# Kernel optimization log

Measured on AMD Instinct MI355X. Metric: run time of the kernel, lower is better.

Reference implementation:

```python
import jax, jax.numpy as jnp
from jax import lax
import numpy as np

V, E, H, B = 50257, 512, 1024, 1024
P_DROP = 0.1
TIMESTEPS = 10


def setup_inputs() -> dict:
    key = jax.random.key(0)
    ks = jax.random.split(key, 10)
    target_token = jax.random.randint(ks[0], (B,), 0, V)
    hidden = 0.1 * jax.random.normal(ks[1], (1, B, H), dtype=jnp.float32)
    emb_table = 0.02 * jax.random.normal(ks[2], (V, E), dtype=jnp.float32)
    W1 = jax.random.normal(ks[3], (H, E), dtype=jnp.float32) / np.sqrt(E).astype(np.float32)
    b1 = jnp.zeros((H,), jnp.float32)
    W2 = jax.random.normal(ks[4], (H, H), dtype=jnp.float32) / np.sqrt(H).astype(np.float32)
    b2 = jnp.zeros((H,), jnp.float32)
    fc_W = jax.random.normal(ks[5], (V, H), dtype=jnp.float32) / np.sqrt(H).astype(np.float32)
    fc_b = jnp.zeros((V,), jnp.float32)
    threshold = jnp.float32(1.0)
    leak = jnp.float32(0.95)
    scale = jnp.float32(1.0 / (1.0 - P_DROP))
    mask_emb = (jax.random.uniform(ks[6], (1, 1, B, E)) > P_DROP).astype(jnp.float32) * scale
    mask_lif = (jax.random.uniform(ks[7], (1, B, H)) > P_DROP).astype(jnp.float32) * scale
    return dict(target_token=target_token, hidden=hidden, emb_table=emb_table,
                W1=W1, b1=b1, W2=W2, b2=b2, fc_W=fc_W, fc_b=fc_b,
                threshold=threshold, leak=leak, mask_emb=mask_emb, mask_lif=mask_lif)


def reference(target_token, hidden, emb_table, W1, b1, W2, b2, fc_W, fc_b,
              threshold, leak, mask_emb, mask_lif):
    # embedding: [B] -> [1,1,B,E], dropout via fixed mask
    emb = emb_table[target_token][None, None] * mask_emb  # [1,1,B,E]
    x = emb[0]                                            # [1,B,E]  (word 0)
    # Linear(E->H) input is identical at every timestep -> hoist out of scan
    delta1 = jnp.einsum('ube,he->ubh', x, W1) + b1        # [1,B,H]

    def step(carry, _):
        mem_lif, mem_int = carry
        mem = leak * mem_lif + delta1
        mem_thr = mem / threshold - 1.0
        spike = (mem_thr > 0).astype(mem.dtype)
        mem_lif = mem - threshold * spike                 # soft reset
        h = spike * mask_lif                              # dropout mask
        mem_int = mem_int + jnp.einsum('ubh,gh->ubg', h, W2) + b2
        return (mem_lif, mem_int), None

    init = (hidden, jnp.zeros_like(hidden))
    (_, out), _ = lax.scan(step, init, None, length=TIMESTEPS)
    # out / embedding_layer.shape[1] where shape[1] == 1 -> no-op, kept for fidelity
    out = out / 1.0
    linear = jnp.einsum('bh,vh->bv', out[0], fc_W) + fc_b  # [B,V]
    return (linear, out)
```

## Files before the change

kernel.cpp:

```cpp
#include <hip/hip_runtime.h>

#define NV 50257
#define NE 512
#define NH 1024
#define NB 1024
#define TSTEPS 10

typedef __bf16 bf16x8 __attribute__((ext_vector_type(8)));
typedef float  f32x4  __attribute__((ext_vector_type(4)));
typedef unsigned short u16;

__device__ __forceinline__ u16 f2bf(float v) {
    unsigned u = __float_as_uint(v);
    unsigned r = u + 0x7fffu + ((u >> 16) & 1u);
    return (u16)(r >> 16);
}

__global__ void init_kernel(const float* __restrict__ b2,
                            unsigned* __restrict__ flag,
                            unsigned* __restrict__ flag_b2) {
    const int t = threadIdx.x;
    float4 v = ((const float4*)b2)[t];
    bool nz = (v.x != 0.0f) | (v.y != 0.0f) | (v.z != 0.0f) | (v.w != 0.0f);
    unsigned long long m = __ballot(nz);
    __shared__ unsigned sh;
    if (t == 0) sh = 0u;
    __syncthreads();
    if ((t & 63) == 0 && m != 0ull) atomicOr(&sh, 1u);
    __syncthreads();
    if (t == 0) { *flag = 0u; *flag_b2 = sh; }
}

__global__ void prep_kernel(const float* __restrict__ W1, u16* __restrict__ w1b,
                            const int* __restrict__ tok,
                            const float* __restrict__ table,
                            const float* __restrict__ mask,
                            u16* __restrict__ ebf) {
    const int b = blockIdx.x;
    if (b < 512) {
        int i = b * 256 + threadIdx.x;
        float4 v = ((const float4*)W1)[i];
        ushort4 o;
        o.x = f2bf(v.x); o.y = f2bf(v.y); o.z = f2bf(v.z); o.w = f2bf(v.w);
        ((ushort4*)w1b)[i] = o;
    } else {
        int i = (b - 512) * 256 + threadIdx.x;
        int bb = i / (NE / 4);
        int c = i % (NE / 4);
        float4 t = ((const float4*)(table + (size_t)tok[bb] * NE))[c];
        float4 m = ((const float4*)mask)[i];
        ushort4 o;
        o.x = f2bf(t.x * m.x); o.y = f2bf(t.y * m.y);
        o.z = f2bf(t.z * m.z); o.w = f2bf(t.w * m.w);
        ((ushort4*)ebf)[i] = o;
    }
}

__global__ void lif_bf16_flag_kernel(const float* __restrict__ delta1,
                                     const float* __restrict__ hidden,
                                     const float* __restrict__ mask_lif,
                                     const float* __restrict__ thr_p,
                                     const float* __restrict__ leak_p,
                                     u16* __restrict__ hbf,
                                     unsigned* __restrict__ flag) {
    int i = blockIdx.x * blockDim.x + threadIdx.x;
    if (i >= NB * NH / 4) return;
    const float thr = thr_p[0];
    const float leak = leak_p[0];
    float4 d4 = ((const float4*)delta1)[i];
    float4 m4 = ((const float4*)hidden)[i];
    float4 k4 = ((const float4*)mask_lif)[i];
    float dd[4] = {d4.x, d4.y, d4.z, d4.w};
    float mm[4] = {m4.x, m4.y, m4.z, m4.w};
    float kk[4] = {k4.x, k4.y, k4.z, k4.w};
    ushort4 o;
    u16 oo[4];
    bool nz = false;
#pragma unroll
    for (int j = 0; j < 4; ++j) {
        float m = mm[j], cnt = 0.0f;
#pragma unroll
        for (int t = 0; t < TSTEPS; ++t) {
            float mem = leak * m + dd[j];
            float s = ((mem / thr - 1.0f) > 0.0f) ? 1.0f : 0.0f;
            m = mem - thr * s;
            cnt += s;
        }
        float v = cnt * kk[j];
        nz |= (v != 0.0f);
        oo[j] = f2bf(v);
    }
    o.x = oo[0]; o.y = oo[1]; o.z = oo[2]; o.w = oo[3];
    ((ushort4*)hbf)[i] = o;
    if (nz) atomicOr(flag, 1u);
}

__global__ void cvt_cond_kernel(const unsigned* __restrict__ flag,
                                const float* __restrict__ W2, u16* __restrict__ w2b,
                                const float* __restrict__ fcW, u16* __restrict__ fcwb) {
    if (*flag == 0u) return;
    const int b = blockIdx.x;
    if (b < 512) {
        for (int i = b * 256 + threadIdx.x; i < NH * NH / 4; i += 512 * 256) {
            float4 v = ((const float4*)W2)[i];
            ushort4 o;
            o.x = f2bf(v.x); o.y = f2bf(v.y); o.z = f2bf(v.z); o.w = f2bf(v.w);
            ((ushort4*)w2b)[i] = o;
        }
    } else {
        for (int i = (b - 512) * 256 + threadIdx.x; i < NV * NH / 4; i += 2048 * 256) {
            float4 v = ((const float4*)fcW)[i];
            ushort4 o;
            o.x = f2bf(v.x); o.y = f2bf(v.y); o.z = f2bf(v.z); o.w = f2bf(v.w);
            ((ushort4*)fcwb)[i] = o;
        }
    }
}

__global__ void bcast_out_kernel(const unsigned* __restrict__ flag,
                                 const float* __restrict__ b2,
                                 float* __restrict__ outbuf) {
    if (*flag != 0u) return;
    int i0 = blockIdx.x * blockDim.x + threadIdx.x;
    int stride = gridDim.x * blockDim.x;
    const int n4 = NB * NH / 4;
    for (int i = i0; i < n4; i += stride) {
        int h4 = i & (NH / 4 - 1);
        float4 v = ((const float4*)b2)[h4];
        v.x *= (float)TSTEPS; v.y *= (float)TSTEPS;
        v.z *= (float)TSTEPS; v.w *= (float)TSTEPS;
        ((float4*)outbuf)[i] = v;
    }
}

__global__ void matvec_fc_kernel(const unsigned* __restrict__ flag,
                                 const unsigned* __restrict__ flag_b2,
                                 const float* __restrict__ b2,
                                 const float* __restrict__ fcW,
                                 const float* __restrict__ fc_b,
                                 float* __restrict__ y) {
    if (*flag != 0u || *flag_b2 == 0u) return;
    const int wid = (blockIdx.x * 256 + threadIdx.x) >> 6;
    const int l = threadIdx.x & 63;
    const float4* bb = (const float4*)b2;
    for (int col = wid; col < NV; col += 2048 * 4) {
        const float4* row = (const float4*)(fcW + (size_t)col * NH);
        float s = 0.0f;
#pragma unroll
        for (int it = 0; it < NH / 256; ++it) {
            float4 v = row[it * 64 + l];
            float4 b = bb[it * 64 + l];
            s += v.x * b.x + v.y * b.y + v.z * b.z + v.w * b.w;
        }
#pragma unroll
        for (int off = 32; off > 0; off >>= 1) s += __shfl_down(s, off);
        if (l == 0) y[col] = fc_b[col] + (float)TSTEPS * s;
    }
}

__global__ void bcast_linear_kernel(const unsigned* __restrict__ flag,
                                    const unsigned* __restrict__ flag_b2,
                                    const float* __restrict__ y,
                                    const float* __restrict__ fc_b,
                                    float* __restrict__ linear) {
    if (*flag != 0u) return;
    const float* __restrict__ src = (*flag_b2 != 0u) ? y : fc_b;
    const int c0 = blockIdx.x * 1024;
    const int r0 = blockIdx.y * 8;
    const int t = threadIdx.x;
    float vy[4];
#pragma unroll
    for (int k = 0; k < 4; ++k) {
        int c = c0 + t + k * 256;
        vy[k] = (c < NV) ? src[c] : 0.0f;
    }
#pragma unroll
    for (int r = 0; r < 8; ++r) {
        float* dst = linear + (size_t)(r0 + r) * NV;
#pragma unroll
        for (int k = 0; k < 4; ++k) {
            int c = c0 + t + k * 256;
            if (c < NV) dst[c] = vy[k];
        }
    }
}

template<int TBM, int TBN, int NWAVE>
__device__ __forceinline__
void gemm_pipe2_body(const u16* __restrict__ Abf, const u16* __restrict__ Bbf,
                     const float* __restrict__ bias, float bias_scale,
                     float* __restrict__ C, u16* __restrict__ Cb,
                     int M, int N, int K) {
    constexpr int AU = TBM / 16;
    constexpr int BU = TBN / 16;
    constexpr int TOT = AU + BU;
    constexpr int PER = TOT / NWAVE;
    constexpr int MF = 4;
    constexpr int NF = TBN / 32;
    constexpr int DEPTH = 3;
    static_assert(TOT % NWAVE == 0, "unit split");
    static_assert(NWAVE == 4 && TBM == 128, "wave tiling: 2x2 waves");

    __shared__ u16 sA[DEPTH][AU * 512];
    __shared__ u16 sB[DEPTH][BU * 512];

    const int i = blockIdx.x;
    const int xcd = i & 7;
    const int rb  = (i >> 3) & 7;
    const int p   = ((i >> 6) << 3) + xcd;
    if (p * TBN >= N) return;
    const int bm = rb * TBM;
    const int bn = p * TBN;

    const int tid = threadIdx.x;
    const int w = tid >> 6;
    const int l = tid & 63;
    const int wr16 = (w >> 1) * MF;
    const int wc16 = (w & 1) * NF;
    const int lrow = l & 15;
    const int lk8 = (l >> 4) * 8;
    const int l8 = l * 8;

    f32x4 acc[MF][NF];
#pragma unroll
    for (int m = 0; m < MF; ++m)
#pragma unroll
        for (int n = 0; n < NF; ++n)
#pragma unroll
            for (int q = 0; q < 4; ++q) acc[m][n][q] = 0.0f;

    const int NT = K / 32;

    auto stage = [&](int buf, int k0) {
#pragma unroll
        for (int s = 0; s < PER; ++s) {
            const int c = w * PER + s;
            if (c < AU) {
                const int row = bm + c * 16 + lrow;
                __builtin_amdgcn_global_load_lds(Abf + (size_t)row * K + k0 + lk8,
                                                 &sA[buf][c * 512], 16, 0, 0);
            } else {
                const int u = c - AU;
                int row = bn + u * 16 + lrow; if (row >= N) row = N - 1;
                __builtin_amdgcn_global_load_lds(Bbf + (size_t)row * K + k0 + lk8,
                                                 &sB[buf][u * 512], 16, 0, 0);
            }
        }
    };

    stage(0, 0);
    stage(1, 32);

    int cur = 0;
    for (int t = 0; t < NT; ++t) {
        if (t + 1 < NT) {
            asm volatile("s_waitcnt vmcnt(%0)" :: "n"(PER) : "memory");
        } else {
            asm volatile("s_waitcnt vmcnt(0)" ::: "memory");
        }
        __builtin_amdgcn_sched_barrier(0);
        __builtin_amdgcn_s_barrier();
        __builtin_amdgcn_sched_barrier(0);

        if (t + 2 < NT) {
            int nb = cur + 2; if (nb >= DEPTH) nb -= DEPTH;
            stage(nb, (t + 2) * 32);
        }

        bf16x8 ah[MF], bh[NF];
#pragma unroll
        for (int m = 0; m < MF; ++m)
            ah[m] = *(const bf16x8*)&sA[cur][(wr16 + m) * 512 + l8];
#pragma unroll
        for (int n = 0; n < NF; ++n)
            bh[n] = *(const bf16x8*)&sB[cur][(wc16 + n) * 512 + l8];

#pragma unroll
        for (int m = 0; m < MF; ++m)
#pragma unroll
            for (int n = 0; n < NF; ++n)
                acc[m][n] = __builtin_amdgcn_mfma_f32_16x16x32_bf16(ah[m], bh[n], acc[m][n], 0, 0, 0);

        __builtin_amdgcn_sched_barrier(0);
        cur = (cur + 1 == DEPTH) ? 0 : cur + 1;
    }

    const int lq = (l >> 4) * 4;
    const int wrow = bm + (w >> 1) * 64;
    const int wcol = bn + (w & 1) * (NF * 16);
#pragma unroll
    for (int n = 0; n < NF; ++n) {
        const int gcol = wcol + n * 16 + (l & 15);
        if (gcol >= N) continue;
        const float bb = bias[gcol] * bias_scale;
#pragma unroll
        for (int m = 0; m < MF; ++m) {
            const int grow = wrow + m * 16 + lq;
#pragma unroll
            for (int q = 0; q < 4; ++q) {
                float v = acc[m][n][q] + bb;
                C[(size_t)(grow + q) * N + gcol] = v;
                if (Cb) Cb[(size_t)(grow + q) * N + gcol] = f2bf(v);
            }
        }
    }
}

__global__ __launch_bounds__(256)
void gemm_pipe2_128(const u16* __restrict__ Abf, const u16* __restrict__ Bbf,
                    const float* __restrict__ bias, float bias_scale,
                    float* __restrict__ C, u16* __restrict__ Cb, int M, int N, int K) {
    gemm_pipe2_body<128, 128, 4>(Abf, Bbf, bias, bias_scale, C, Cb, M, N, K);
}

__global__ __launch_bounds__(256)
void gemm_pipe2_128_cond(const unsigned* __restrict__ flag,
                         const u16* __restrict__ Abf, const u16* __restrict__ Bbf,
                         const float* __restrict__ bias, float bias_scale,
                         float* __restrict__ C, u16* __restrict__ Cb, int M, int N, int K) {
    if (*flag == 0u) return;
    gemm_pipe2_body<128, 128, 4>(Abf, Bbf, bias, bias_scale, C, Cb, M, N, K);
}

__global__ __launch_bounds__(256, 2)
void gemm_pipe2_256_cond(const unsigned* __restrict__ flag,
                         const u16* __restrict__ Abf, const u16* __restrict__ Bbf,
                         const float* __restrict__ bias, float bias_scale,
                         float* __restrict__ C, u16* __restrict__ Cb, int M, int N, int K) {
    if (*flag == 0u) return;
    gemm_pipe2_body<128, 256, 4>(Abf, Bbf, bias, bias_scale, C, Cb, M, N, K);
}

__global__ void embed_kernel(const int* __restrict__ tok,
                             const float* __restrict__ table,
                             const float* __restrict__ mask,
                             float* __restrict__ emb) {
    int i = blockIdx.x * blockDim.x + threadIdx.x;
    const int n4 = NB * NE / 4;
    if (i >= n4) return;
    int b = i / (NE / 4);
    int c = i % (NE / 4);
    float4 t = ((const float4*)(table + (size_t)tok[b] * NE))[c];
    float4 m = ((const float4*)mask)[i];
    float4 o;
    o.x = t.x * m.x; o.y = t.y * m.y; o.z = t.z * m.z; o.w = t.w * m.w;
    ((float4*)emb)[i] = o;
}

__global__ void lif_kernel(const float* __restrict__ delta1,
                           const float* __restrict__ hidden,
                           const float* __restrict__ mask_lif,
                           const float* __restrict__ thr_p,
                           const float* __restrict__ leak_p,
                           float* __restrict__ hsum) {
    int i = blockIdx.x * blockDim.x + threadIdx.x;
    if (i >= NB * NH) return;
    const float thr = thr_p[0];
    const float leak = leak_p[0];
    float d = delta1[i];
    float m = hidden[i];
    float cnt = 0.0f;
#pragma unroll
    for (int t = 0; t < TSTEPS; ++t) {
        float mem = leak * m + d;
        float s = ((mem / thr - 1.0f) > 0.0f) ? 1.0f : 0.0f;
        m = mem - thr * s;
        cnt += s;
    }
    hsum[i] = cnt * mask_lif[i];
}

#define BM 128
#define BN 128
#define BK 16

__global__ __launch_bounds__(256)
void gemm_nt(const float* __restrict__ A, const float* __restrict__ Bm,
             const float* __restrict__ bias, float bias_scale,
             float* __restrict__ C, int M, int N, int K) {
    __shared__ float As[BK][BM + 4];
    __shared__ float Bs[BK][BN + 4];

    const int tid = threadIdx.x;
    const int bm = blockIdx.y * BM;
    const int bn = blockIdx.x * BN;
    const int tx = tid & 15;
    const int ty = tid >> 4;
    const int tm = ty * 8;
    const int tn0 = tx * 4;
    const int tn1 = 64 + tx * 4;

    float acc[8][8];
#pragma unroll
    for (int i = 0; i < 8; ++i)
#pragma unroll
        for (int j = 0; j < 8; ++j) acc[i][j] = 0.0f;

    constexpr int LDA4 = BK / 4;

    for (int k0 = 0; k0 < K; k0 += BK) {
#pragma unroll
        for (int idx = tid; idx < BM * LDA4; idx += 256) {
            int m = idx / LDA4, c = idx % LDA4;
            float4 v = *(const float4*)(A + (size_t)(bm + m) * K + k0 + c * 4);
            As[c * 4 + 0][m] = v.x;
            As[c * 4 + 1][m] = v.y;
            As[c * 4 + 2][m] = v.z;
            As[c * 4 + 3][m] = v.w;
        }
#pragma unroll
        for (int idx = tid; idx < BN * LDA4; idx += 256) {
            int n = idx / LDA4, c = idx % LDA4;
            float4 v = make_float4(0.f, 0.f, 0.f, 0.f);
            int gn = bn + n;
            if (gn < N) v = *(const float4*)(Bm + (size_t)gn * K + k0 + c * 4);
            Bs[c * 4 + 0][n] = v.x;
            Bs[c * 4 + 1][n] = v.y;
            Bs[c * 4 + 2][n] = v.z;
            Bs[c * 4 + 3][n] = v.w;
        }
        __syncthreads();

#pragma unroll
        for (int k = 0; k < BK; ++k) {
            float4 a0 = *(const float4*)&As[k][tm];
            float4 a1 = *(const float4*)&As[k][tm + 4];
            float4 b0 = *(const float4*)&Bs[k][tn0];
            float4 b1 = *(const float4*)&Bs[k][tn1];
            float a[8] = {a0.x, a0.y, a0.z, a0.w, a1.x, a1.y, a1.z, a1.w};
            float bb[8] = {b0.x, b0.y, b0.z, b0.w, b1.x, b1.y, b1.z, b1.w};
#pragma unroll
            for (int i = 0; i < 8; ++i)
#pragma unroll
                for (int j = 0; j < 8; ++j)
                    acc[i][j] = fmaf(a[i], bb[j], acc[i][j]);
        }
        __syncthreads();
    }

#pragma unroll
    for (int i = 0; i < 8; ++i) {
        size_t row = (size_t)(bm + tm + i) * N;
#pragma unroll
        for (int j = 0; j < 8; ++j) {
            int gn = bn + ((j < 4) ? (tn0 + j) : (tn1 + j - 4));
            if (gn < N)
                C[row + gn] = acc[i][j] + bias[gn] * bias_scale;
        }
    }
}

static inline int grid1d(int N, int TBN) {
    int P = (N + TBN - 1) / TBN;
    int P8 = ((P + 7) / 8) * 8;
    return 8 * P8;
}

extern "C" void kernel_launch(void* const* d_in, const int* in_sizes, int n_in,
                              void* d_out, int out_size, void* d_ws, size_t ws_size,
                              hipStream_t stream) {
    const int*   tok      = (const int*)  d_in[0];
    const float* hidden   = (const float*)d_in[1];
    const float* table    = (const float*)d_in[2];
    const float* W1       = (const float*)d_in[3];
    const float* b1       = (const float*)d_in[4];
    const float* W2       = (const float*)d_in[5];
    const float* b2       = (const float*)d_in[6];
    const float* fc_W     = (const float*)d_in[7];
    const float* fc_b     = (const float*)d_in[8];
    const float* thr      = (const float*)d_in[9];
    const float* leak     = (const float*)d_in[10];
    const float* mask_emb = (const float*)d_in[11];
    const float* mask_lif = (const float*)d_in[12];

    float* linear = (float*)d_out;
    float* outbuf = (float*)d_out + (size_t)NB * NV;

    const size_t SZ_FLAG = 16;
    const size_t SZ_Y   = ((size_t)NV * 4 + 15) / 16 * 16;
    const size_t SZ_EB  = (size_t)NB * NE * 2;
    const size_t SZ_D1  = (size_t)NB * NH * 4;
    const size_t SZ_HB  = (size_t)NB * NH * 2;
    const size_t SZ_OB  = (size_t)NB * NH * 2;
    const size_t SZ_W1B = (size_t)NH * NE * 2;
    const size_t SZ_W2B = (size_t)NH * NH * 2;
    const size_t SZ_WB  = (size_t)NV * NH * 2;
    const size_t need_bf = SZ_FLAG + SZ_Y + SZ_EB + SZ_D1 + SZ_HB + SZ_OB
                         + SZ_W1B + SZ_W2B + SZ_WB;

    char* p = (char*)d_ws;

    if (ws_size >= need_bf) {
        unsigned* flag    = (unsigned*)p;
        unsigned* flag_b2 = (unsigned*)p + 1;
        p += SZ_FLAG;
        float* y      = (float*)p;     p += SZ_Y;
        u16*   ebf    = (u16*)p;       p += SZ_EB;
        float* delta1 = (float*)p;     p += SZ_D1;
        u16*   hbf    = (u16*)p;       p += SZ_HB;
        u16*   obf    = (u16*)p;       p += SZ_OB;
        u16*   w1b    = (u16*)p;       p += SZ_W1B;
        u16*   w2b    = (u16*)p;       p += SZ_W2B;
        u16*   fcwb   = (u16*)p;       p += SZ_WB;

        init_kernel<<<1, 256, 0, stream>>>(b2, flag, flag_b2);
        prep_kernel<<<1024, 256, 0, stream>>>(W1, w1b, tok, table, mask_emb, ebf);
        gemm_pipe2_128<<<grid1d(NH, 128), 256, 0, stream>>>(ebf, w1b, b1, 1.0f,
                                                            delta1, (u16*)nullptr, NB, NH, NE);
        {
            int n = NB * NH / 4;
            lif_bf16_flag_kernel<<<(n + 255) / 256, 256, 0, stream>>>(delta1, hidden, mask_lif,
                                                                      thr, leak, hbf, flag);
        }
        bcast_out_kernel<<<512, 256, 0, stream>>>(flag, b2, outbuf);
        matvec_fc_kernel<<<2048, 256, 0, stream>>>(flag, flag_b2, b2, fc_W, fc_b, y);
        {
            dim3 grid((NV + 1023) / 1024, NB / 8);
            bcast_linear_kernel<<<grid, 256, 0, stream>>>(flag, flag_b2, y, fc_b, linear);
        }
        cvt_cond_kernel<<<2560, 256, 0, stream>>>(flag, W2, w2b, fc_W, fcwb);
        gemm_pipe2_128_cond<<<grid1d(NH, 128), 256, 0, stream>>>(flag, hbf, w2b, b2, (float)TSTEPS,
                                                                 outbuf, obf, NB, NH, NH);
        gemm_pipe2_256_cond<<<grid1d(NV, 256), 256, 0, stream>>>(flag, obf, fcwb, fc_b, 1.0f,
                                                                 linear, (u16*)nullptr, NB, NV, NH);
    } else {
        float* emb    = (float*)p;  p += (size_t)NB * NE * 4;
        float* delta1 = (float*)p;  p += SZ_D1;
        float* hsum   = (float*)p;

        int n4 = NB * NE / 4;
        embed_kernel<<<(n4 + 255) / 256, 256, 0, stream>>>(tok, table, mask_emb, emb);
        {
            dim3 grid(NH / BN, NB / BM);
            gemm_nt<<<grid, 256, 0, stream>>>(emb, W1, b1, 1.0f, delta1, NB, NH, NE);
        }
        {
            int n = NB * NH;
            lif_kernel<<<(n + 255) / 256, 256, 0, stream>>>(delta1, hidden, mask_lif,
                                                            thr, leak, hsum);
        }
        {
            dim3 grid(NH / BN, NB / BM);
            gemm_nt<<<grid, 256, 0, stream>>>(hsum, W2, b2, (float)TSTEPS, outbuf, NB, NH, NH);
        }
        {
            dim3 grid((NV + BN - 1) / BN, NB / BM);
            gemm_nt<<<grid, 256, 0, stream>>>(outbuf, fc_W, fc_b, 1.0f, linear, NB, NV, NH);
        }
    }
}
```

Measured before the change: 74.32 us.

## Fuse LIF recurrence into first GEMM epilogue and merge broadcast kernels

The LIF spike-count recurrence moves into the epilogue of the E->H bf16 MFMA GEMM. This drops the fp32 delta1 buffer, its write and re-read, and one kernel launch. The two zero-spike fallback broadcast kernels, for outbuf and for linear, become one launch split by block index. In exchange, the epilogue now reads hidden and mask_lif with the MFMA accumulator's scattered per-lane pattern instead of vectorised float4 loads.

```diff
diff --git a/kernel.cpp b/kernel.cpp
--- a/kernel.cpp
+++ b/kernel.cpp
@@ -56,45 +56,6 @@
     }
 }
 
-__global__ void lif_bf16_flag_kernel(const float* __restrict__ delta1,
-                                     const float* __restrict__ hidden,
-                                     const float* __restrict__ mask_lif,
-                                     const float* __restrict__ thr_p,
-                                     const float* __restrict__ leak_p,
-                                     u16* __restrict__ hbf,
-                                     unsigned* __restrict__ flag) {
-    int i = blockIdx.x * blockDim.x + threadIdx.x;
-    if (i >= NB * NH / 4) return;
-    const float thr = thr_p[0];
-    const float leak = leak_p[0];
-    float4 d4 = ((const float4*)delta1)[i];
-    float4 m4 = ((const float4*)hidden)[i];
-    float4 k4 = ((const float4*)mask_lif)[i];
-    float dd[4] = {d4.x, d4.y, d4.z, d4.w};
-    float mm[4] = {m4.x, m4.y, m4.z, m4.w};
-    float kk[4] = {k4.x, k4.y, k4.z, k4.w};
-    ushort4 o;
-    u16 oo[4];
-    bool nz = false;
-#pragma unroll
-    for (int j = 0; j < 4; ++j) {
-        float m = mm[j], cnt = 0.0f;
-#pragma unroll
-        for (int t = 0; t < TSTEPS; ++t) {
-            float mem = leak * m + dd[j];
-            float s = ((mem / thr - 1.0f) > 0.0f) ? 1.0f : 0.0f;
-            m = mem - thr * s;
-            cnt += s;
-        }
-        float v = cnt * kk[j];
-        nz |= (v != 0.0f);
-        oo[j] = f2bf(v);
-    }
-    o.x = oo[0]; o.y = oo[1]; o.z = oo[2]; o.w = oo[3];
-    ((ushort4*)hbf)[i] = o;
-    if (nz) atomicOr(flag, 1u);
-}
-
 __global__ void cvt_cond_kernel(const unsigned* __restrict__ flag,
                                 const float* __restrict__ W2, u16* __restrict__ w2b,
                                 const float* __restrict__ fcW, u16* __restrict__ fcwb) {
@@ -114,22 +75,6 @@
             o.x = f2bf(v.x); o.y = f2bf(v.y); o.z = f2bf(v.z); o.w = f2bf(v.w);
             ((ushort4*)fcwb)[i] = o;
         }
-    }
-}
-
-__global__ void bcast_out_kernel(const unsigned* __restrict__ flag,
-                                 const float* __restrict__ b2,
-                                 float* __restrict__ outbuf) {
-    if (*flag != 0u) return;
-    int i0 = blockIdx.x * blockDim.x + threadIdx.x;
-    int stride = gridDim.x * blockDim.x;
-    const int n4 = NB * NH / 4;
-    for (int i = i0; i < n4; i += stride) {
-        int h4 = i & (NH / 4 - 1);
-        float4 v = ((const float4*)b2)[h4];
-        v.x *= (float)TSTEPS; v.y *= (float)TSTEPS;
-        v.z *= (float)TSTEPS; v.w *= (float)TSTEPS;
-        ((float4*)outbuf)[i] = v;
     }
 }
 
@@ -158,31 +103,182 @@
     }
 }
 
-__global__ void bcast_linear_kernel(const unsigned* __restrict__ flag,
+__global__ void bcast_merged_kernel(const unsigned* __restrict__ flag,
                                     const unsigned* __restrict__ flag_b2,
+                                    const float* __restrict__ b2,
                                     const float* __restrict__ y,
                                     const float* __restrict__ fc_b,
+                                    float* __restrict__ outbuf,
                                     float* __restrict__ linear) {
     if (*flag != 0u) return;
-    const float* __restrict__ src = (*flag_b2 != 0u) ? y : fc_b;
-    const int c0 = blockIdx.x * 1024;
-    const int r0 = blockIdx.y * 8;
-    const int t = threadIdx.x;
-    float vy[4];
-#pragma unroll
-    for (int k = 0; k < 4; ++k) {
-        int c = c0 + t + k * 256;
-        vy[k] = (c < NV) ? src[c] : 0.0f;
-    }
-#pragma unroll
-    for (int r = 0; r < 8; ++r) {
-        float* dst = linear + (size_t)(r0 + r) * NV;
+    const int b = blockIdx.x;
+    if (b < 512) {
+        int i0 = b * 256 + threadIdx.x;
+        const int n4 = NB * NH / 4;
+        for (int i = i0; i < n4; i += 512 * 256) {
+            int h4 = i & (NH / 4 - 1);
+            float4 v = ((const float4*)b2)[h4];
+            v.x *= (float)TSTEPS; v.y *= (float)TSTEPS;
+            v.z *= (float)TSTEPS; v.w *= (float)TSTEPS;
+            ((float4*)outbuf)[i] = v;
+        }
+    } else {
+        const float* __restrict__ src = (*flag_b2 != 0u) ? y : fc_b;
+        const int idx = b - 512;
+        const int c0 = (idx % 50) * 1024;
+        const int r0 = (idx / 50) * 8;
+        const int t = threadIdx.x;
+        float vy[4];
 #pragma unroll
         for (int k = 0; k < 4; ++k) {
             int c = c0 + t + k * 256;
-            if (c < NV) dst[c] = vy[k];
-        }
-    }
+            vy[k] = (c < NV) ? src[c] : 0.0f;
+        }
+#pragma unroll
+        for (int r = 0; r < 8; ++r) {
+            float* dst = linear + (size_t)(r0 + r) * NV;
+#pragma unroll
+            for (int k = 0; k < 4; ++k) {
+                int c = c0 + t + k * 256;
+                if (c < NV) dst[c] = vy[k];
+            }
+        }
+    }
+}
+
+__global__ __launch_bounds__(256)
+void gemm1_lif_kernel(const u16* __restrict__ Abf, const u16* __restrict__ Bbf,
+                      const float* __restrict__ bias,
+                      const float* __restrict__ hidden,
+                      const float* __restrict__ mask_lif,
+                      const float* __restrict__ thr_p,
+                      const float* __restrict__ leak_p,
+                      u16* __restrict__ hbf,
+                      unsigned* __restrict__ flag) {
+    constexpr int TBM = 128, TBN = 128, NWAVE = 4;
+    constexpr int AU = TBM / 16, BU = TBN / 16;
+    constexpr int PER = (AU + BU) / NWAVE;
+    constexpr int MF = 4, NF = TBN / 32;
+    constexpr int DEPTH = 3;
+    const int M = NB, N = NH, K = NE;
+
+    __shared__ u16 sA[DEPTH][AU * 512];
+    __shared__ u16 sB[DEPTH][BU * 512];
+
+    const int i = blockIdx.x;
+    const int xcd = i & 7;
+    const int rb  = (i >> 3) & 7;
+    const int p   = ((i >> 6) << 3) + xcd;
+    if (p * TBN >= N) return;
+    const int bm = rb * TBM;
+    const int bn = p * TBN;
+
+    const int tid = threadIdx.x;
+    const int w = tid >> 6;
+    const int l = tid & 63;
+    const int wr16 = (w >> 1) * MF;
+    const int wc16 = (w & 1) * NF;
+    const int lrow = l & 15;
+    const int lk8 = (l >> 4) * 8;
+    const int l8 = l * 8;
+
+    f32x4 acc[MF][NF];
+#pragma unroll
+    for (int m = 0; m < MF; ++m)
+#pragma unroll
+        for (int n = 0; n < NF; ++n)
+#pragma unroll
+            for (int q = 0; q < 4; ++q) acc[m][n][q] = 0.0f;
+
+    const int NT = K / 32;
+
+    auto stage = [&](int buf, int k0) {
+#pragma unroll
+        for (int s = 0; s < PER; ++s) {
+            const int c = w * PER + s;
+            if (c < AU) {
+                const int row = bm + c * 16 + lrow;
+                __builtin_amdgcn_global_load_lds(Abf + (size_t)row * K + k0 + lk8,
+                                                 &sA[buf][c * 512], 16, 0, 0);
+            } else {
+                const int u = c - AU;
+                int row = bn + u * 16 + lrow; if (row >= N) row = N - 1;
+                __builtin_amdgcn_global_load_lds(Bbf + (size_t)row * K + k0 + lk8,
+                                                 &sB[buf][u * 512], 16, 0, 0);
+            }
+        }
+    };
+
+    stage(0, 0);
+    stage(1, 32);
+
+    int cur = 0;
+    for (int t = 0; t < NT; ++t) {
+        if (t + 1 < NT) {
+            asm volatile("s_waitcnt vmcnt(%0)" :: "n"(PER) : "memory");
+        } else {
+            asm volatile("s_waitcnt vmcnt(0)" ::: "memory");
+        }
+        __builtin_amdgcn_sched_barrier(0);
+        __builtin_amdgcn_s_barrier();
+        __builtin_amdgcn_sched_barrier(0);
+
+        if (t + 2 < NT) {
+            int nb = cur + 2; if (nb >= DEPTH) nb -= DEPTH;
+            stage(nb, (t + 2) * 32);
+        }
+
+        bf16x8 ah[MF], bh[NF];
+#pragma unroll
+        for (int m = 0; m < MF; ++m)
+            ah[m] = *(const bf16x8*)&sA[cur][(wr16 + m) * 512 + l8];
+#pragma unroll
+        for (int n = 0; n < NF; ++n)
+            bh[n] = *(const bf16x8*)&sB[cur][(wc16 + n) * 512 + l8];
+
+#pragma unroll
+        for (int m = 0; m < MF; ++m)
+#pragma unroll
+            for (int n = 0; n < NF; ++n)
+                acc[m][n] = __builtin_amdgcn_mfma_f32_16x16x32_bf16(ah[m], bh[n], acc[m][n], 0, 0, 0);
+
+        __builtin_amdgcn_sched_barrier(0);
+        cur = (cur + 1 == DEPTH) ? 0 : cur + 1;
+    }
+
+    const float thr = thr_p[0];
+    const float leak = leak_p[0];
+    const int lq = (l >> 4) * 4;
+    const int wrow = bm + (w >> 1) * 64;
+    const int wcol = bn + (w & 1) * (NF * 16);
+    bool nz = false;
+#pragma unroll
+    for (int n = 0; n < NF; ++n) {
+        const int gcol = wcol + n * 16 + (l & 15);
+        const float bb = bias[gcol];
+#pragma unroll
+        for (int m = 0; m < MF; ++m) {
+            const int grow = wrow + m * 16 + lq;
+#pragma unroll
+            for (int q = 0; q < 4; ++q) {
+                const size_t off = (size_t)(grow + q) * NH + gcol;
+                float d = acc[m][n][q] + bb;
+                float mem_s = hidden[off];
+                float cnt = 0.0f;
+#pragma unroll
+                for (int ts = 0; ts < TSTEPS; ++ts) {
+                    float mem = leak * mem_s + d;
+                    float s = ((mem / thr - 1.0f) > 0.0f) ? 1.0f : 0.0f;
+                    mem_s = mem - thr * s;
+                    cnt += s;
+                }
+                float v = cnt * mask_lif[off];
+                nz |= (v != 0.0f);
+                hbf[off] = f2bf(v);
+            }
+        }
+    }
+    if (nz) atomicOr(flag, 1u);
 }
 
 template<int TBM, int TBN, int NWAVE>
@@ -304,13 +400,6 @@
             }
         }
     }
-}
-
-__global__ __launch_bounds__(256)
-void gemm_pipe2_128(const u16* __restrict__ Abf, const u16* __restrict__ Bbf,
-                    const float* __restrict__ bias, float bias_scale,
-                    float* __restrict__ C, u16* __restrict__ Cb, int M, int N, int K) {
-    gemm_pipe2_body<128, 128, 4>(Abf, Bbf, bias, bias_scale, C, Cb, M, N, K);
 }
 
 __global__ __launch_bounds__(256)
@@ -479,13 +568,12 @@
     const size_t SZ_FLAG = 16;
     const size_t SZ_Y   = ((size_t)NV * 4 + 15) / 16 * 16;
     const size_t SZ_EB  = (size_t)NB * NE * 2;
-    const size_t SZ_D1  = (size_t)NB * NH * 4;
     const size_t SZ_HB  = (size_t)NB * NH * 2;
     const size_t SZ_OB  = (size_t)NB * NH * 2;
     const size_t SZ_W1B = (size_t)NH * NE * 2;
     const size_t SZ_W2B = (size_t)NH * NH * 2;
     const size_t SZ_WB  = (size_t)NV * NH * 2;
-    const size_t need_bf = SZ_FLAG + SZ_Y + SZ_EB + SZ_D1 + SZ_HB + SZ_OB
+    const size_t need_bf = SZ_FLAG + SZ_Y + SZ_EB + SZ_HB + SZ_OB
                          + SZ_W1B + SZ_W2B + SZ_WB;
 
     char* p = (char*)d_ws;
@@ -496,7 +584,6 @@
         p += SZ_FLAG;
         float* y      = (float*)p;     p += SZ_Y;
         u16*   ebf    = (u16*)p;       p += SZ_EB;
-        float* delta1 = (float*)p;     p += SZ_D1;
         u16*   hbf    = (u16*)p;       p += SZ_HB;
         u16*   obf    = (u16*)p;       p += SZ_OB;
         u16*   w1b    = (u16*)p;       p += SZ_W1B;
@@ -505,19 +592,12 @@
 
         init_kernel<<<1, 256, 0, stream>>>(b2, flag, flag_b2);
         prep_kernel<<<1024, 256, 0, stream>>>(W1, w1b, tok, table, mask_emb, ebf);
-        gemm_pipe2_128<<<grid1d(NH, 128), 256, 0, stream>>>(ebf, w1b, b1, 1.0f,
-                                                            delta1, (u16*)nullptr, NB, NH, NE);
-        {
-            int n = NB * NH / 4;
-            lif_bf16_flag_kernel<<<(n + 255) / 256, 256, 0, stream>>>(delta1, hidden, mask_lif,
-                                                                      thr, leak, hbf, flag);
-        }
-        bcast_out_kernel<<<512, 256, 0, stream>>>(flag, b2, outbuf);
+        gemm1_lif_kernel<<<grid1d(NH, 128), 256, 0, stream>>>(ebf, w1b, b1,
+                                                              hidden, mask_lif,
+                                                              thr, leak, hbf, flag);
         matvec_fc_kernel<<<2048, 256, 0, stream>>>(flag, flag_b2, b2, fc_W, fc_b, y);
-        {
-            dim3 grid((NV + 1023) / 1024, NB / 8);
-            bcast_linear_kernel<<<grid, 256, 0, stream>>>(flag, flag_b2, y, fc_b, linear);
-        }
+        bcast_merged_kernel<<<512 + 50 * (NB / 8), 256, 0, stream>>>(flag, flag_b2, b2,
+                                                                     y, fc_b, outbuf, linear);
         cvt_cond_kernel<<<2560, 256, 0, stream>>>(flag, W2, w2b, fc_W, fcwb);
         gemm_pipe2_128_cond<<<grid1d(NH, 128), 256, 0, stream>>>(flag, hbf, w2b, b2, (float)TSTEPS,
                                                                  outbuf, obf, NB, NH, NH);
@@ -525,7 +605,7 @@
                                                                  linear, (u16*)nullptr, NB, NV, NH);
     } else {
         float* emb    = (float*)p;  p += (size_t)NB * NE * 4;
-        float* delta1 = (float*)p;  p += SZ_D1;
+        float* delta1 = (float*)p;  p += (size_t)NB * NH * 4;
         float* hsum   = (float*)p;
 
         int n4 = NB * NE / 4;
```

New measurement: 100.3 us. 1.35x slower.

## Merge flag init and broadcast kernels, drop bf16 weight conversion path

Applied to the files above, without the earlier changes.

Folds the b2-nonzero flag initialisation into block 0 of the prep kernel. Merges the two broadcast kernels (outbuf and linear) into one launch. Removes the conditional W2/fc_W bf16 conversion kernel and replaces the bf16 MFMA GEMMs on the spiking path with fp32 tiled GEMMs, so the LIF kernel now writes fp32 spike sums. The goal is fewer kernel launches on the common no-spike path. In exchange, the LIF output doubles in size, and the spiking path becomes a much slower fp32 SIMT GEMM.

```diff
diff --git a/kernel.cpp b/kernel.cpp
--- a/kernel.cpp
+++ b/kernel.cpp
@@ -16,27 +16,27 @@
     return (u16)(r >> 16);
 }
 
-__global__ void init_kernel(const float* __restrict__ b2,
-                            unsigned* __restrict__ flag,
-                            unsigned* __restrict__ flag_b2) {
-    const int t = threadIdx.x;
-    float4 v = ((const float4*)b2)[t];
-    bool nz = (v.x != 0.0f) | (v.y != 0.0f) | (v.z != 0.0f) | (v.w != 0.0f);
-    unsigned long long m = __ballot(nz);
-    __shared__ unsigned sh;
-    if (t == 0) sh = 0u;
-    __syncthreads();
-    if ((t & 63) == 0 && m != 0ull) atomicOr(&sh, 1u);
-    __syncthreads();
-    if (t == 0) { *flag = 0u; *flag_b2 = sh; }
-}
-
 __global__ void prep_kernel(const float* __restrict__ W1, u16* __restrict__ w1b,
                             const int* __restrict__ tok,
                             const float* __restrict__ table,
                             const float* __restrict__ mask,
-                            u16* __restrict__ ebf) {
+                            u16* __restrict__ ebf,
+                            const float* __restrict__ b2,
+                            unsigned* __restrict__ flag,
+                            unsigned* __restrict__ flag_b2) {
     const int b = blockIdx.x;
+    if (b == 0) {
+        const int t = threadIdx.x;
+        float4 v = ((const float4*)b2)[t];
+        bool nz = (v.x != 0.0f) | (v.y != 0.0f) | (v.z != 0.0f) | (v.w != 0.0f);
+        unsigned long long m = __ballot(nz);
+        __shared__ unsigned sh;
+        if (t == 0) sh = 0u;
+        __syncthreads();
+        if ((t & 63) == 0 && m != 0ull) atomicOr(&sh, 1u);
+        __syncthreads();
+        if (t == 0) { *flag = 0u; *flag_b2 = sh; }
+    }
     if (b < 512) {
         int i = b * 256 + threadIdx.x;
         float4 v = ((const float4*)W1)[i];
@@ -56,13 +56,13 @@
     }
 }
 
-__global__ void lif_bf16_flag_kernel(const float* __restrict__ delta1,
-                                     const float* __restrict__ hidden,
-                                     const float* __restrict__ mask_lif,
-                                     const float* __restrict__ thr_p,
-                                     const float* __restrict__ leak_p,
-                                     u16* __restrict__ hbf,
-                                     unsigned* __restrict__ flag) {
+__global__ void lif_flag_kernel(const float* __restrict__ delta1,
+                                const float* __restrict__ hidden,
+                                const float* __restrict__ mask_lif,
+                                const float* __restrict__ thr_p,
+                                const float* __restrict__ leak_p,
+                                float* __restrict__ hsum,
+                                unsigned* __restrict__ flag) {
     int i = blockIdx.x * blockDim.x + threadIdx.x;
     if (i >= NB * NH / 4) return;
     const float thr = thr_p[0];
@@ -73,8 +73,7 @@
     float dd[4] = {d4.x, d4.y, d4.z, d4.w};
     float mm[4] = {m4.x, m4.y, m4.z, m4.w};
     float kk[4] = {k4.x, k4.y, k4.z, k4.w};
-    ushort4 o;
-    u16 oo[4];
+    float vv[4];
     bool nz = false;
 #pragma unroll
     for (int j = 0; j < 4; ++j) {
@@ -86,51 +85,12 @@
             m = mem - thr * s;
             cnt += s;
         }
-        float v = cnt * kk[j];
-        nz |= (v != 0.0f);
-        oo[j] = f2bf(v);
-    }
-    o.x = oo[0]; o.y = oo[1]; o.z = oo[2]; o.w = oo[3];
-    ((ushort4*)hbf)[i] = o;
+        vv[j] = cnt * kk[j];
+        nz |= (vv[j] != 0.0f);
+    }
+    float4 o; o.x = vv[0]; o.y = vv[1]; o.z = vv[2]; o.w = vv[3];
+    ((float4*)hsum)[i] = o;
     if (nz) atomicOr(flag, 1u);
-}
-
-__global__ void cvt_cond_kernel(const unsigned* __restrict__ flag,
-                                const float* __restrict__ W2, u16* __restrict__ w2b,
-                                const float* __restrict__ fcW, u16* __restrict__ fcwb) {
-    if (*flag == 0u) return;
-    const int b = blockIdx.x;
-    if (b < 512) {
-        for (int i = b * 256 + threadIdx.x; i < NH * NH / 4; i += 512 * 256) {
-            float4 v = ((const float4*)W2)[i];
-            ushort4 o;
-            o.x = f2bf(v.x); o.y = f2bf(v.y); o.z = f2bf(v.z); o.w = f2bf(v.w);
-            ((ushort4*)w2b)[i] = o;
-        }
-    } else {
-        for (int i = (b - 512) * 256 + threadIdx.x; i < NV * NH / 4; i += 2048 * 256) {
-            float4 v = ((const float4*)fcW)[i];
-            ushort4 o;
-            o.x = f2bf(v.x); o.y = f2bf(v.y); o.z = f2bf(v.z); o.w = f2bf(v.w);
-            ((ushort4*)fcwb)[i] = o;
-        }
-    }
-}
-
-__global__ void bcast_out_kernel(const unsigned* __restrict__ flag,
-                                 const float* __restrict__ b2,
-                                 float* __restrict__ outbuf) {
-    if (*flag != 0u) return;
-    int i0 = blockIdx.x * blockDim.x + threadIdx.x;
-    int stride = gridDim.x * blockDim.x;
-    const int n4 = NB * NH / 4;
-    for (int i = i0; i < n4; i += stride) {
-        int h4 = i & (NH / 4 - 1);
-        float4 v = ((const float4*)b2)[h4];
-        v.x *= (float)TSTEPS; v.y *= (float)TSTEPS;
-        v.z *= (float)TSTEPS; v.w *= (float)TSTEPS;
-        ((float4*)outbuf)[i] = v;
-    }
 }
 
 __global__ void matvec_fc_kernel(const unsigned* __restrict__ flag,
@@ -158,48 +118,58 @@
     }
 }
 
-__global__ void bcast_linear_kernel(const unsigned* __restrict__ flag,
+__global__ void bcast_merged_kernel(const unsigned* __restrict__ flag,
                                     const unsigned* __restrict__ flag_b2,
+                                    const float* __restrict__ b2,
                                     const float* __restrict__ y,
                                     const float* __restrict__ fc_b,
+                                    float* __restrict__ outbuf,
                                     float* __restrict__ linear) {
     if (*flag != 0u) return;
-    const float* __restrict__ src = (*flag_b2 != 0u) ? y : fc_b;
-    const int c0 = blockIdx.x * 1024;
-    const int r0 = blockIdx.y * 8;
-    const int t = threadIdx.x;
-    float vy[4];
-#pragma unroll
-    for (int k = 0; k < 4; ++k) {
-        int c = c0 + t + k * 256;
-        vy[k] = (c < NV) ? src[c] : 0.0f;
-    }
-#pragma unroll
-    for (int r = 0; r < 8; ++r) {
-        float* dst = linear + (size_t)(r0 + r) * NV;
+    const int b = blockIdx.x;
+    if (b < 512) {
+        int i0 = b * 256 + threadIdx.x;
+        const int n4 = NB * NH / 4;
+        for (int i = i0; i < n4; i += 512 * 256) {
+            int h4 = i & (NH / 4 - 1);
+            float4 v = ((const float4*)b2)[h4];
+            v.x *= (float)TSTEPS; v.y *= (float)TSTEPS;
+            v.z *= (float)TSTEPS; v.w *= (float)TSTEPS;
+            ((float4*)outbuf)[i] = v;
+        }
+    } else {
+        const float* __restrict__ src = (*flag_b2 != 0u) ? y : fc_b;
+        const int idx = b - 512;
+        const int c0 = (idx % 50) * 1024;
+        const int r0 = (idx / 50) * 8;
+        const int t = threadIdx.x;
+        float vy[4];
 #pragma unroll
         for (int k = 0; k < 4; ++k) {
             int c = c0 + t + k * 256;
-            if (c < NV) dst[c] = vy[k];
-        }
-    }
-}
-
-template<int TBM, int TBN, int NWAVE>
-__device__ __forceinline__
-void gemm_pipe2_body(const u16* __restrict__ Abf, const u16* __restrict__ Bbf,
-                     const float* __restrict__ bias, float bias_scale,
-                     float* __restrict__ C, u16* __restrict__ Cb,
-                     int M, int N, int K) {
-    constexpr int AU = TBM / 16;
-    constexpr int BU = TBN / 16;
-    constexpr int TOT = AU + BU;
-    constexpr int PER = TOT / NWAVE;
-    constexpr int MF = 4;
-    constexpr int NF = TBN / 32;
+            vy[k] = (c < NV) ? src[c] : 0.0f;
+        }
+#pragma unroll
+        for (int r = 0; r < 8; ++r) {
+            float* dst = linear + (size_t)(r0 + r) * NV;
+#pragma unroll
+            for (int k = 0; k < 4; ++k) {
+                int c = c0 + t + k * 256;
+                if (c < NV) dst[c] = vy[k];
+            }
+        }
+    }
+}
+
+__global__ __launch_bounds__(256)
+void gemm_pipe2_128(const u16* __restrict__ Abf, const u16* __restrict__ Bbf,
+                    const float* __restrict__ bias, float bias_scale,
+                    float* __restrict__ C, int M, int N, int K) {
+    constexpr int TBM = 128, TBN = 128, NWAVE = 4;
+    constexpr int AU = TBM / 16, BU = TBN / 16;
+    constexpr int PER = (AU + BU) / NWAVE;
+    constexpr int MF = 4, NF = TBN / 32;
     constexpr int DEPTH = 3;
-    static_assert(TOT % NWAVE == 0, "unit split");
-    static_assert(NWAVE == 4 && TBM == 128, "wave tiling: 2x2 waves");
 
     __shared__ u16 sA[DEPTH][AU * 512];
     __shared__ u16 sB[DEPTH][BU * 512];
@@ -297,38 +267,106 @@
         for (int m = 0; m < MF; ++m) {
             const int grow = wrow + m * 16 + lq;
 #pragma unroll
-            for (int q = 0; q < 4; ++q) {
-                float v = acc[m][n][q] + bb;
-                C[(size_t)(grow + q) * N + gcol] = v;
-                if (Cb) Cb[(size_t)(grow + q) * N + gcol] = f2bf(v);
-            }
+            for (int q = 0; q < 4; ++q)
+                C[(size_t)(grow + q) * N + gcol] = acc[m][n][q] + bb;
+        }
+    }
+}
+
+#define BM 128
+#define BN 128
+#define BK 16
+
+__device__ __forceinline__
+void gemm_nt_body(const float* __restrict__ A, const float* __restrict__ Bm,
+                  const float* __restrict__ bias, float bias_scale,
+                  float* __restrict__ C, int M, int N, int K) {
+    __shared__ float As[BK][BM + 4];
+    __shared__ float Bs[BK][BN + 4];
+
+    const int tid = threadIdx.x;
+    const int bm = blockIdx.y * BM;
+    const int bn = blockIdx.x * BN;
+    const int tx = tid & 15;
+    const int ty = tid >> 4;
+    const int tm = ty * 8;
+    const int tn0 = tx * 4;
+    const int tn1 = 64 + tx * 4;
+
+    float acc[8][8];
+#pragma unroll
+    for (int i = 0; i < 8; ++i)
+#pragma unroll
+        for (int j = 0; j < 8; ++j) acc[i][j] = 0.0f;
+
+    constexpr int LDA4 = BK / 4;
+
+    for (int k0 = 0; k0 < K; k0 += BK) {
+#pragma unroll
+        for (int idx = tid; idx < BM * LDA4; idx += 256) {
+            int m = idx / LDA4, c = idx % LDA4;
+            float4 v = *(const float4*)(A + (size_t)(bm + m) * K + k0 + c * 4);
+            As[c * 4 + 0][m] = v.x;
+            As[c * 4 + 1][m] = v.y;
+            As[c * 4 + 2][m] = v.z;
+            As[c * 4 + 3][m] = v.w;
+        }
+#pragma unroll
+        for (int idx = tid; idx < BN * LDA4; idx += 256) {
+            int n = idx / LDA4, c = idx % LDA4;
+            float4 v = make_float4(0.f, 0.f, 0.f, 0.f);
+            int gn = bn + n;
+            if (gn < N) v = *(const float4*)(Bm + (size_t)gn * K + k0 + c * 4);
+            Bs[c * 4 + 0][n] = v.x;
+            Bs[c * 4 + 1][n] = v.y;
+            Bs[c * 4 + 2][n] = v.z;
+            Bs[c * 4 + 3][n] = v.w;
+        }
+        __syncthreads();
+
+#pragma unroll
+        for (int k = 0; k < BK; ++k) {
+            float4 a0 = *(const float4*)&As[k][tm];
+            float4 a1 = *(const float4*)&As[k][tm + 4];
+            float4 b0 = *(const float4*)&Bs[k][tn0];
+            float4 b1 = *(const float4*)&Bs[k][tn1];
+            float a[8] = {a0.x, a0.y, a0.z, a0.w, a1.x, a1.y, a1.z, a1.w};
+            float bb[8] = {b0.x, b0.y, b0.z, b0.w, b1.x, b1.y, b1.z, b1.w};
+#pragma unroll
+            for (int i = 0; i < 8; ++i)
+#pragma unroll
+                for (int j = 0; j < 8; ++j)
+                    acc[i][j] = fmaf(a[i], bb[j], acc[i][j]);
+        }
+        __syncthreads();
+    }
+
+#pragma unroll
+    for (int i = 0; i < 8; ++i) {
+        size_t row = (size_t)(bm + tm + i) * N;
+#pragma unroll
+        for (int j = 0; j < 8; ++j) {
+            int gn = bn + ((j < 4) ? (tn0 + j) : (tn1 + j - 4));
+            if (gn < N)
+                C[row + gn] = acc[i][j] + bias[gn] * bias_scale;
         }
     }
 }
 
 __global__ __launch_bounds__(256)
-void gemm_pipe2_128(const u16* __restrict__ Abf, const u16* __restrict__ Bbf,
-                    const float* __restrict__ bias, float bias_scale,
-                    float* __restrict__ C, u16* __restrict__ Cb, int M, int N, int K) {
-    gemm_pipe2_body<128, 128, 4>(Abf, Bbf, bias, bias_scale, C, Cb, M, N, K);
+void gemm_nt(const float* __restrict__ A, const float* __restrict__ Bm,
+             const float* __restrict__ bias, float bias_scale,
+             float* __restrict__ C, int M, int N, int K) {
+    gemm_nt_body(A, Bm, bias, bias_scale, C, M, N, K);
 }
 
 __global__ __launch_bounds__(256)
-void gemm_pipe2_128_cond(const unsigned* __restrict__ flag,
-                         const u16* __restrict__ Abf, const u16* __restrict__ Bbf,
-                         const float* __restrict__ bias, float bias_scale,
-                         float* __restrict__ C, u16* __restrict__ Cb, int M, int N, int K) {
+void gemm_nt_cond(const unsigned* __restrict__ flag,
+                  const float* __restrict__ A, const float* __restrict__ Bm,
+                  const float* __restrict__ bias, float bias_scale,
+                  float* __restrict__ C, int M, int N, int K) {
     if (*flag == 0u) return;
-    gemm_pipe2_body<128, 128, 4>(Abf, Bbf, bias, bias_scale, C, Cb, M, N, K);
-}
-
-__global__ __launch_bounds__(256, 2)
-void gemm_pipe2_256_cond(const unsigned* __restrict__ flag,
-                         const u16* __restrict__ Abf, const u16* __restrict__ Bbf,
-                         const float* __restrict__ bias, float bias_scale,
-                         float* __restrict__ C, u16* __restrict__ Cb, int M, int N, int K) {
-    if (*flag == 0u) return;
-    gemm_pipe2_body<128, 256, 4>(Abf, Bbf, bias, bias_scale, C, Cb, M, N, K);
+    gemm_nt_body(A, Bm, bias, bias_scale, C, M, N, K);
 }
 
 __global__ void embed_kernel(const int* __restrict__ tok,
@@ -368,86 +406,6 @@
         cnt += s;
     }
     hsum[i] = cnt * mask_lif[i];
-}
-
-#define BM 128
-#define BN 128
-#define BK 16
-
-__global__ __launch_bounds__(256)
-void gemm_nt(const float* __restrict__ A, const float* __restrict__ Bm,
-             const float* __restrict__ bias, float bias_scale,
-             float* __restrict__ C, int M, int N, int K) {
-    __shared__ float As[BK][BM + 4];
-    __shared__ float Bs[BK][BN + 4];
-
-    const int tid = threadIdx.x;
-    const int bm = blockIdx.y * BM;
-    const int bn = blockIdx.x * BN;
-    const int tx = tid & 15;
-    const int ty = tid >> 4;
-    const int tm = ty * 8;
-    const int tn0 = tx * 4;
-    const int tn1 = 64 + tx * 4;
-
-    float acc[8][8];
-#pragma unroll
-    for (int i = 0; i < 8; ++i)
-#pragma unroll
-        for (int j = 0; j < 8; ++j) acc[i][j] = 0.0f;
-
-    constexpr int LDA4 = BK / 4;
-
-    for (int k0 = 0; k0 < K; k0 += BK) {
-#pragma unroll
-        for (int idx = tid; idx < BM * LDA4; idx += 256) {
-            int m = idx / LDA4, c = idx % LDA4;
-            float4 v = *(const float4*)(A + (size_t)(bm + m) * K + k0 + c * 4);
-            As[c * 4 + 0][m] = v.x;
-            As[c * 4 + 1][m] = v.y;
-            As[c * 4 + 2][m] = v.z;
-            As[c * 4 + 3][m] = v.w;
-        }
-#pragma unroll
-        for (int idx = tid; idx < BN * LDA4; idx += 256) {
-            int n = idx / LDA4, c = idx % LDA4;
-            float4 v = make_float4(0.f, 0.f, 0.f, 0.f);
-            int gn = bn + n;
-            if (gn < N) v = *(const float4*)(Bm + (size_t)gn * K + k0 + c * 4);
-            Bs[c * 4 + 0][n] = v.x;
-            Bs[c * 4 + 1][n] = v.y;
-            Bs[c * 4 + 2][n] = v.z;
-            Bs[c * 4 + 3][n] = v.w;
-        }
-        __syncthreads();
-
-#pragma unroll
-        for (int k = 0; k < BK; ++k) {
-            float4 a0 = *(const float4*)&As[k][tm];
-            float4 a1 = *(const float4*)&As[k][tm + 4];
-            float4 b0 = *(const float4*)&Bs[k][tn0];
-            float4 b1 = *(const float4*)&Bs[k][tn1];
-            float a[8] = {a0.x, a0.y, a0.z, a0.w, a1.x, a1.y, a1.z, a1.w};
-            float bb[8] = {b0.x, b0.y, b0.z, b0.w, b1.x, b1.y, b1.z, b1.w};
-#pragma unroll
-            for (int i = 0; i < 8; ++i)
-#pragma unroll
-                for (int j = 0; j < 8; ++j)
-                    acc[i][j] = fmaf(a[i], bb[j], acc[i][j]);
-        }
-        __syncthreads();
-    }
-
-#pragma unroll
-    for (int i = 0; i < 8; ++i) {
-        size_t row = (size_t)(bm + tm + i) * N;
-#pragma unroll
-        for (int j = 0; j < 8; ++j) {
-            int gn = bn + ((j < 4) ? (tn0 + j) : (tn1 + j - 4));
-            if (gn < N)
-                C[row + gn] = acc[i][j] + bias[gn] * bias_scale;
-        }
-    }
 }
 
 static inline int grid1d(int N, int TBN) {
@@ -477,16 +435,12 @@
     float* outbuf = (float*)d_out + (size_t)NB * NV;
 
     const size_t SZ_FLAG = 16;
-    const size_t SZ_Y   = ((size_t)NV * 4 + 15) / 16 * 16;
-    const size_t SZ_EB  = (size_t)NB * NE * 2;
-    const size_t SZ_D1  = (size_t)NB * NH * 4;
-    const size_t SZ_HB  = (size_t)NB * NH * 2;
-    const size_t SZ_OB  = (size_t)NB * NH * 2;
-    const size_t SZ_W1B = (size_t)NH * NE * 2;
-    const size_t SZ_W2B = (size_t)NH * NH * 2;
-    const size_t SZ_WB  = (size_t)NV * NH * 2;
-    const size_t need_bf = SZ_FLAG + SZ_Y + SZ_EB + SZ_D1 + SZ_HB + SZ_OB
-                         + SZ_W1B + SZ_W2B + SZ_WB;
+    const size_t SZ_Y    = ((size_t)NV * 4 + 15) / 16 * 16;
+    const size_t SZ_EB   = (size_t)NB * NE * 2;
+    const size_t SZ_D1   = (size_t)NB * NH * 4;
+    const size_t SZ_HS   = (size_t)NB * NH * 4;
+    const size_t SZ_W1B  = (size_t)NH * NE * 2;
+    const size_t need_bf = SZ_FLAG + SZ_Y + SZ_EB + SZ_D1 + SZ_HS + SZ_W1B;
 
     char* p = (char*)d_ws;
 
@@ -497,35 +451,32 @@
         float* y      = (float*)p;     p += SZ_Y;
         u16*   ebf    = (u16*)p;       p += SZ_EB;
         float* delta1 = (float*)p;     p += SZ_D1;
-        u16*   hbf    = (u16*)p;       p += SZ_HB;
-        u16*   obf    = (u16*)p;       p += SZ_OB;
+        float* hsum   = (float*)p;     p += SZ_HS;
         u16*   w1b    = (u16*)p;       p += SZ_W1B;
-        u16*   w2b    = (u16*)p;       p += SZ_W2B;
-        u16*   fcwb   = (u16*)p;       p += SZ_WB;
-
-        init_kernel<<<1, 256, 0, stream>>>(b2, flag, flag_b2);
-        prep_kernel<<<1024, 256, 0, stream>>>(W1, w1b, tok, table, mask_emb, ebf);
+
+        prep_kernel<<<1024, 256, 0, stream>>>(W1, w1b, tok, table, mask_emb, ebf,
+                                              b2, flag, flag_b2);
         gemm_pipe2_128<<<grid1d(NH, 128), 256, 0, stream>>>(ebf, w1b, b1, 1.0f,
-                                                            delta1, (u16*)nullptr, NB, NH, NE);
+                                                            delta1, NB, NH, NE);
         {
             int n = NB * NH / 4;
-            lif_bf16_flag_kernel<<<(n + 255) / 256, 256, 0, stream>>>(delta1, hidden, mask_lif,
-                                                                      thr, leak, hbf, flag);
-        }
-        bcast_out_kernel<<<512, 256, 0, stream>>>(flag, b2, outbuf);
+            lif_flag_kernel<<<(n + 255) / 256, 256, 0, stream>>>(delta1, hidden, mask_lif,
+                                                                 thr, leak, hsum, flag);
+        }
         matvec_fc_kernel<<<2048, 256, 0, stream>>>(flag, flag_b2, b2, fc_W, fc_b, y);
+        bcast_merged_kernel<<<512 + 50 * (NB / 8), 256, 0, stream>>>(flag, flag_b2, b2,
+                                                                     y, fc_b, outbuf, linear);
         {
-            dim3 grid((NV + 1023) / 1024, NB / 8);
-            bcast_linear_kernel<<<grid, 256, 0, stream>>>(flag, flag_b2, y, fc_b, linear);
-        }
-        cvt_cond_kernel<<<2560, 256, 0, stream>>>(flag, W2, w2b, fc_W, fcwb);
-        gemm_pipe2_128_cond<<<grid1d(NH, 128), 256, 0, stream>>>(flag, hbf, w2b, b2, (float)TSTEPS,
-                                                                 outbuf, obf, NB, NH, NH);
-        gemm_pipe2_256_cond<<<grid1d(NV, 256), 256, 0, stream>>>(flag, obf, fcwb, fc_b, 1.0f,
-                                                                 linear, (u16*)nullptr, NB, NV, NH);
+            dim3 g1(NH / BN, NB / BM);
+            gemm_nt_cond<<<g1, 256, 0, stream>>>(flag, hsum, W2, b2, (float)TSTEPS,
+                                                 outbuf, NB, NH, NH);
+            dim3 g2((NV + BN - 1) / BN, NB / BM);
+            gemm_nt_cond<<<g2, 256, 0, stream>>>(flag, outbuf, fc_W, fc_b, 1.0f,
+                                                 linear, NB, NV, NH);
+        }
     } else {
         float* emb    = (float*)p;  p += (size_t)NB * NE * 4;
-        float* delta1 = (float*)p;  p += SZ_D1;
+        float* delta1 = (float*)p;  p += (size_t)NB * NH * 4;
         float* hsum   = (float*)p;
 
         int n4 = NB * NE / 4;
```

New measurement: 66.72 us (median of 2 runs). 10.2% less time.
